# Optimization experiments

Measured on AMD Instinct MI355X. Metric: run time of the kernel, lower is better.

The kernel has to match this reference:

```python
import jax, jax.numpy as jnp
import numpy as np


def _lstm_scan(x, W, U, b):
    """Unidirectional Keras-style LSTM over x: [B, T, F] -> [B, T, H].
    Gate order (i, f, c, o); sigmoid recurrent activation, tanh activation."""
    B = x.shape[0]
    H = U.shape[0]
    # Precompute input projections for all timesteps: [B, T, 4H]
    xp = jnp.einsum('btf,fg->btg', x, W) + b

    def step(carry, xt):
        h, c = carry
        z = xt + h @ U  # [B, 4H]
        i, f, g, o = jnp.split(z, 4, axis=-1)
        i = jax.nn.sigmoid(i)
        f = jax.nn.sigmoid(f)
        g = jnp.tanh(g)
        o = jax.nn.sigmoid(o)
        c = f * c + i * g
        h = o * jnp.tanh(c)
        return (h, c), h

    init = (jnp.zeros((B, H), x.dtype), jnp.zeros((B, H), x.dtype))
    _, hs = jax.lax.scan(step, init, xp.transpose(1, 0, 2))  # [T, B, H]
    return hs.transpose(1, 0, 2)


def _bidir(x, Wf, Uf, bf, Wb, Ub, bb):
    fwd = _lstm_scan(x, Wf, Uf, bf)
    bwd = jnp.flip(_lstm_scan(jnp.flip(x, axis=1), Wb, Ub, bb), axis=1)
    return jnp.concatenate([fwd, bwd], axis=-1)  # merge_mode='concat'


def setup_inputs() -> dict:
    key = jax.random.key(0)
    ks = jax.random.split(key, 16)
    B, T, F, H = 64, 1024, 64, 256
    s_in0 = 1.0 / np.sqrt(F)
    s_in1 = 1.0 / np.sqrt(2 * H)
    s_rec = 1.0 / np.sqrt(H)
    inp = {
        'x': jax.random.normal(ks[0], (B, T, F), jnp.float32),
        'W0f': jax.random.normal(ks[1], (F, 4 * H), jnp.float32) * s_in0,
        'U0f': jax.random.normal(ks[2], (H, 4 * H), jnp.float32) * s_rec,
        'b0f': jnp.zeros((4 * H,), jnp.float32),
        'W0b': jax.random.normal(ks[3], (F, 4 * H), jnp.float32) * s_in0,
        'U0b': jax.random.normal(ks[4], (H, 4 * H), jnp.float32) * s_rec,
        'b0b': jnp.zeros((4 * H,), jnp.float32),
        'W1f': jax.random.normal(ks[5], (2 * H, 4 * H), jnp.float32) * s_in1,
        'U1f': jax.random.normal(ks[6], (H, 4 * H), jnp.float32) * s_rec,
        'b1f': jnp.zeros((4 * H,), jnp.float32),
        'W1b': jax.random.normal(ks[7], (2 * H, 4 * H), jnp.float32) * s_in1,
        'U1b': jax.random.normal(ks[8], (H, 4 * H), jnp.float32) * s_rec,
        'b1b': jnp.zeros((4 * H,), jnp.float32),
        'Wd': jax.random.normal(ks[9], (2 * H, 1), jnp.float32) * s_in1,
        'bd': jnp.zeros((1,), jnp.float32),
    }
    return inp


def reference(x, W0f, U0f, b0f, W0b, U0b, b0b,
              W1f, U1f, b1f, W1b, U1b, b1b, Wd, bd):
    # Layer 0 bidirectional LSTM -> [B, T, 2H]; dropout is identity at inference
    h = _bidir(x, W0f, U0f, b0f, W0b, U0b, b0b)
    # Layer 1 bidirectional LSTM -> [B, T, 2H]
    h = _bidir(h, W1f, U1f, b1f, W1b, U1b, b1b)
    # Dense(1, linear) head -> [B, T, 1]
    return jnp.einsum('btd,do->bto', h, Wd) + bd
```

## Files before the change

kernel.cpp:

```cpp
#include <hip/hip_runtime.h>
#include <hip/hip_bf16.h>
#include <cstdint>
#include <cstddef>

#define B_ 64
#define T_ 1024

typedef _Float16 half_t;
typedef __attribute__((ext_vector_type(8))) _Float16 half8;
typedef __attribute__((ext_vector_type(4))) float f32x4;
typedef __attribute__((ext_vector_type(8))) unsigned short ushort8;

__device__ __forceinline__ float sigm(float x) { return 1.f / (1.f + __expf(-x)); }
__device__ __forceinline__ float tanh_fast(float x) {
  float e = __expf(2.f * x);
  return 1.f - 2.f / (e + 1.f);
}

__global__ __launch_bounds__(256) void permute_cols(const float* __restrict__ src,
                                                    float* __restrict__ dst, int K) {
  int idx = blockIdx.x * 256 + threadIdx.x;
  if (idx >= K * 1024) return;
  int n = idx & 1023;
  size_t k = (size_t)(idx >> 10);
  dst[idx] = src[(k << 10) + ((size_t)(n & 3) << 8) + (n >> 2)];
}

__global__ __launch_bounds__(256) void pack_u_mfma(const float* __restrict__ src,
                                                   half_t* __restrict__ dst) {
  int tid = blockIdx.x * 256 + threadIdx.x;
  int l = tid & 63;
  int s = (tid >> 6) & 7;
  int n = (tid >> 9) & 1;
  int w = (tid >> 10) & 3;
  int wgc = (tid >> 12) & 7;
  int col = wgc * 128 + w * 32 + n * 16 + (l & 15);
  int hc = col >> 2, g = col & 3;
  int k0 = s * 32 + (l >> 4) * 8;
  half8 v;
#pragma unroll
  for (int j = 0; j < 8; ++j)
    v[j] = (half_t)src[(size_t)(k0 + j) * 1024 + (g << 8) + hc];
  *(half8*)(dst + (size_t)tid * 8) = v;
}

__global__ __launch_bounds__(256) void pack_w0_mfma(const float* __restrict__ src,
                                                    half_t* __restrict__ dst) {
  int line = blockIdx.x * 256 + threadIdx.x;
  int l = line & 63;
  int ks = (line >> 6) & 1;
  int n = (line >> 7) & 1;
  int w = (line >> 8) & 3;
  int wgc = (line >> 10) & 7;
  int col = wgc * 128 + w * 32 + n * 16 + (l & 15);
  int sc = ((col & 3) << 8) + (col >> 2);
  int k0 = ks * 32 + (l >> 4) * 8;
  half8 v;
#pragma unroll
  for (int j = 0; j < 8; ++j)
    v[j] = (half_t)src[(size_t)(k0 + j) * 1024 + sc];
  *(half8*)(dst + (size_t)line * 8) = v;
}

__global__ __launch_bounds__(256) void pack_w1_mfma(const float* __restrict__ src,
                                                    half_t* __restrict__ dst) {
  int tid = blockIdx.x * 256 + threadIdx.x;
  int l = tid & 63;
  int ks = (tid >> 6) & 15;
  int nb = tid >> 10;
  int colp = nb * 16 + (l & 15);
  int sc = ((colp & 3) << 8) + (colp >> 2);
  int k0 = ks * 32 + (l >> 4) * 8;
  half8 v;
#pragma unroll
  for (int j = 0; j < 8; ++j)
    v[j] = (half_t)src[(size_t)(k0 + j) * 1024 + sc];
  *(half8*)(dst + (size_t)tid * 8) = v;
}

__global__ __launch_bounds__(256) void pack_x_f16(const float* __restrict__ x,
                                                  unsigned short* __restrict__ xi) {
  int idx = blockIdx.x * 256 + threadIdx.x;
  int b = idx & 15;
  int q = (idx >> 4) & 3;
  int ks = (idx >> 6) & 1;
  int t = (idx >> 7) & 1023;
  int bg = idx >> 17;
  const float* src = x + ((size_t)(bg * 16 + b) * T_ + t) * 64 + ks * 32 + q * 8;
  ushort8 v;
#pragma unroll
  for (int j = 0; j < 8; ++j) {
    half_t h = (half_t)src[j];
    v[j] = __builtin_bit_cast(unsigned short, h);
  }
  *(ushort8*)(xi + (size_t)idx * 8) = v;
}

__global__ __launch_bounds__(256) void init_out(float* __restrict__ out,
                                                const float* __restrict__ bd, int n) {
  int i = blockIdx.x * 256 + threadIdx.x;
  if (i < n) out[i] = bd[0];
}

__global__ __launch_bounds__(256) void diag_out(float* __restrict__ out, int n, float v) {
  int i = blockIdx.x * 256 + threadIdx.x;
  if (i < n) out[i] = (i == 0) ? v : 0.f;
}

__global__ __launch_bounds__(256) void proj1_mfma(
    const unsigned short* __restrict__ h0,
    const half_t* __restrict__ Wf, const half_t* __restrict__ Wb,
    const float* __restrict__ bpf, const float* __restrict__ bpb,
    float* __restrict__ xp, int s0, int Tc) {
  const int dir = blockIdx.z;
  const half_t* Wpk = dir ? Wb : Wf;
  const float* bs = dir ? bpb : bpf;
  const int b = blockIdx.y;
  const int mt = blockIdx.x;
  const int tid = threadIdx.x;
  const int l = tid & 63, w = tid >> 6;

  __shared__ __align__(16) unsigned short A_lds[16][520];

  {
    int r = tid >> 4, c16 = tid & 15;
    int sl = mt * 16 + r;
    int t = dir ? (T_ - 1 - s0 - sl) : (s0 + sl);
    const ushort8* srcp =
        (const ushort8*)(h0 + ((size_t)b * T_ + t) * 512 + c16 * 32);
#pragma unroll
    for (int u = 0; u < 4; ++u)
      *(ushort8*)&A_lds[r][c16 * 32 + u * 8] = srcp[u];
  }
  __syncthreads();

  f32x4 acc[16];
#pragma unroll
  for (int n = 0; n < 16; ++n) acc[n] = (f32x4){0.f, 0.f, 0.f, 0.f};

  for (int ks = 0; ks < 16; ++ks) {
    half8 a = *(const half8*)&A_lds[l & 15][ks * 32 + (l >> 4) * 8];
    const half_t* bp_ = Wpk + (((size_t)(w * 16) * 16 + ks) * 64 + l) * 8;
#pragma unroll
    for (int n = 0; n < 16; ++n) {
      half8 bfr = *(const half8*)(bp_ + (size_t)n * 16 * 64 * 8);
      acc[n] = __builtin_amdgcn_mfma_f32_16x16x32_f16(a, bfr, acc[n], 0, 0, 0);
    }
  }

#pragma unroll
  for (int n = 0; n < 16; ++n) {
    int col = (w * 16 + n) * 16 + (l & 15);
    float bias = bs[col];
#pragma unroll
    for (int r = 0; r < 4; ++r) {
      int sl = mt * 16 + (l >> 4) * 4 + r;
      xp[(((size_t)dir * B_ + b) * Tc + sl) * 1024 + col] = acc[n][r] + bias;
    }
  }
}

template <int L0>
__global__ __launch_bounds__(256, 1) void lstm_scan_mfma(
    const float* __restrict__ xp,
    const unsigned short* __restrict__ xi,
    const half_t* __restrict__ W0f_, const half_t* __restrict__ W0b_,
    const float* __restrict__ b0f_, const float* __restrict__ b0b_,
    const half_t* __restrict__ Upk_f, const half_t* __restrict__ Upk_b,
    float* __restrict__ carry_c,
    unsigned* __restrict__ payl, unsigned* __restrict__ flagw,
    int s0, int Tc, int tagbase,
    unsigned short* __restrict__ hout,
    const float* __restrict__ Wd, float* __restrict__ out) {
  const int blk = blockIdx.x;
  const int unit = blk & 7;
  const int wgc = blk >> 3;
  const int dir = unit & 1;
  const int bg = unit >> 1;
  const int b0u = bg * 16;
  const int tid = threadIdx.x;
  const int l = tid & 63;
  const int w = tid >> 6;

  __shared__ __align__(16) unsigned short A_lds[4096];
  __shared__ __align__(16) unsigned short hstage[512];
  __shared__ float red_sm[64];

  const half_t* Upk = dir ? Upk_b : Upk_f;
  half8 U[2][8];
  {
    const half_t* up = Upk + (size_t)(wgc * 4 + w) * 8192;
#pragma unroll
    for (int n = 0; n < 2; ++n)
#pragma unroll
      for (int s = 0; s < 8; ++s)
        U[n][s] = *(const half8*)(up + ((size_t)(n * 8 + s) * 64 + l) * 8);
  }

  const int b_lane = 4 * (l >> 4) + (l & 3);
  const int hcb = wgc * 32 + w * 8 + ((l >> 2) & 3);
  const int colb = wgc * 128 + w * 32 + (l & 15);
  float cst[2];
#pragma unroll
  for (int n = 0; n < 2; ++n)
    cst[n] = (s0 == 0) ? 0.f
        : carry_c[((size_t)dir * B_ + b0u + b_lane) * 256 + hcb + n * 4];

  float wdl[2] = {0.f, 0.f};
  half8 W0r[2][2];
  float bias0[2] = {0.f, 0.f};
  const unsigned short* xib = nullptr;
  if (L0) {
    const half_t* W0pk = dir ? W0b_ : W0f_;
    const float* bs0 = dir ? b0b_ : b0f_;
#pragma unroll
    for (int n = 0; n < 2; ++n) {
      bias0[n] = bs0[colb + n * 16];
#pragma unroll
      for (int ks = 0; ks < 2; ++ks)
        W0r[n][ks] = *(const half8*)(W0pk +
            ((size_t)(((wgc * 4 + w) * 2 + n) * 2 + ks) * 64 + l) * 8);
    }
    xib = xi + (size_t)bg * T_ * 1024;
  } else {
    wdl[0] = Wd[dir * 256 + hcb];
    wdl[1] = Wd[dir * 256 + hcb + 4];
  }

  unsigned* payl_u = payl + (size_t)unit * 4096;
  unsigned* flag_u = flagw + unit * 16;

  if (s0 == 0) {
#pragma unroll
    for (int i = 0; i < 8; ++i) ((unsigned*)A_lds)[tid * 8 + i] = 0u;
  } else {
    unsigned dd[8];
#pragma unroll
    for (int i = 0; i < 8; ++i)
      dd[i] = __hip_atomic_load(payl_u + 2048 + tid * 8 + i,
                                __ATOMIC_RELAXED, __HIP_MEMORY_SCOPE_AGENT);
#pragma unroll
    for (int i = 0; i < 8; ++i)
      ((unsigned*)A_lds)[tid * 8 + i] = dd[i];
  }
  __syncthreads();

  const float* xpu = L0 ? nullptr : (xp + (size_t)(dir * B_ + b0u) * Tc * 1024);

  float xpre[2][4];
  half8 xfre[2];
  {
    if (L0) {
      int t0f = dir ? (T_ - 1 - s0) : s0;
#pragma unroll
      for (int ks = 0; ks < 2; ++ks)
        xfre[ks] = *(const half8*)((const half_t*)xib + (size_t)t0f * 1024 +
                                   ((ks * 4 + (l >> 4)) * 16 + (l & 15)) * 8);
    } else {
#pragma unroll
      for (int n = 0; n < 2; ++n)
#pragma unroll
        for (int r = 0; r < 4; ++r)
          xpre[n][r] = xpu[((size_t)(4 * (l >> 4) + r) * Tc) * 1024 + colb + n * 16];
    }
  }

  const int hbl = (w * 16 + b_lane) * 8 + ((l >> 2) & 3);

  for (int sl = 0; sl < Tc; ++sl) {
    const int s = s0 + sl;
    const int t = dir ? (T_ - 1 - s) : s;
    const int slot = s & 1;

    f32x4 acc[2];
    if (L0) {
#pragma unroll
      for (int n = 0; n < 2; ++n)
#pragma unroll
        for (int r = 0; r < 4; ++r) acc[n][r] = bias0[n];
      half8 xa0 = xfre[0], xa1 = xfre[1];
#pragma unroll
      for (int n = 0; n < 2; ++n) {
        acc[n] = __builtin_amdgcn_mfma_f32_16x16x32_f16(xa0, W0r[n][0], acc[n], 0, 0, 0);
        acc[n] = __builtin_amdgcn_mfma_f32_16x16x32_f16(xa1, W0r[n][1], acc[n], 0, 0, 0);
      }
    } else {
#pragma unroll
      for (int n = 0; n < 2; ++n)
#pragma unroll
        for (int r = 0; r < 4; ++r) acc[n][r] = xpre[n][r];
    }

    half8 a[8];
#pragma unroll
    for (int sK = 0; sK < 8; ++sK)
      a[sK] = *(const half8*)&((const half_t*)A_lds)[((sK * 4 + (l >> 4)) * 16 + (l & 15)) * 8];

#pragma unroll
    for (int sK = 0; sK < 8; ++sK) {
      acc[0] = __builtin_amdgcn_mfma_f32_16x16x32_f16(a[sK], U[0][sK], acc[0], 0, 0, 0);
      acc[1] = __builtin_amdgcn_mfma_f32_16x16x32_f16(a[sK], U[1][sK], acc[1], 0, 0, 0);
    }

    float vhead = 0.f;
    unsigned short hu2[2];
#pragma unroll
    for (int n = 0; n < 2; ++n) {
      float v0 = acc[n][0], v1 = acc[n][1], v2 = acc[n][2], v3 = acc[n][3];
      float x0 = __shfl_xor(v1, 1), x1 = __shfl_xor(v0, 1);
      float x2 = __shfl_xor(v3, 1), x3 = __shfl_xor(v2, 1);
      float a0 = (l & 1) ? x0 : v0;
      float a1 = (l & 1) ? v1 : x1;
      float a2 = (l & 1) ? x2 : v2;
      float a3 = (l & 1) ? v3 : x3;
      float y0 = __shfl_xor(a2, 2), y1 = __shfl_xor(a3, 2);
      float y2 = __shfl_xor(a0, 2), y3 = __shfl_xor(a1, 2);
      float u0 = (l & 2) ? y0 : a0;
      float u1 = (l & 2) ? y1 : a1;
      float u2 = (l & 2) ? a2 : y2;
      float u3 = (l & 2) ? a3 : y3;

      float iG = sigm(u0), fG = sigm(u1), gG = tanh_fast(u2), oG = sigm(u3);
      float cn = fG * cst[n] + iG * gG;
      cst[n] = cn;
      float h = oG * tanh_fast(cn);

      if (!L0) vhead += h * wdl[n];
      hu2[n] = __builtin_bit_cast(unsigned short, (half_t)h);
      if (sl == Tc - 1)
        carry_c[((size_t)dir * B_ + b0u + b_lane) * 256 + hcb + n * 4] = cn;
    }
    hstage[hbl] = hu2[0];
    hstage[hbl + 4] = hu2[1];
    if (!L0) {
      vhead += __shfl_xor(vhead, 4);
      vhead += __shfl_xor(vhead, 8);
      if ((l & 12) == 0) red_sm[w * 16 + b_lane] = vhead;
    }
    __syncthreads();

    const unsigned* hs32 = (const unsigned*)hstage;
    __hip_atomic_store(payl_u + slot * 2048 + wgc * 256 + tid, hs32[tid],
                       __ATOMIC_RELAXED, __HIP_MEMORY_SCOPE_AGENT);

    asm volatile("s_waitcnt vmcnt(0)" ::: "memory");
    __syncthreads();
    const unsigned want = (unsigned)(tagbase + s + 1);
    if (tid == 0)
      __hip_atomic_store(flag_u + slot * 8 + wgc, want,
                         __ATOMIC_RELAXED, __HIP_MEMORY_SCOPE_AGENT);

    if (L0) {
      int bb = tid >> 4, cc = tid & 15;
      ((unsigned*)hout)[((size_t)(b0u + bb) * T_ + t) * 256 + dir * 128 +
                        wgc * 16 + cc] = hs32[(cc >> 2) * 64 + bb * 4 + (cc & 3)];
    } else if (tid < 16) {
      atomicAdd(out + (((size_t)(b0u + tid)) << 10) + t,
                (red_sm[tid] + red_sm[16 + tid]) +
                (red_sm[32 + tid] + red_sm[48 + tid]));
    }

    if (sl + 1 < Tc) {
      if (L0) {
        int tn = dir ? (T_ - 2 - s) : (s + 1);
#pragma unroll
        for (int ks = 0; ks < 2; ++ks)
          xfre[ks] = *(const half8*)((const half_t*)xib + (size_t)tn * 1024 +
                                     ((ks * 4 + (l >> 4)) * 16 + (l & 15)) * 8);
      } else {
#pragma unroll
        for (int n = 0; n < 2; ++n)
#pragma unroll
          for (int r = 0; r < 4; ++r)
            xpre[n][r] = xpu[((size_t)(4 * (l >> 4) + r) * Tc + sl + 1) * 1024 + colb + n * 16];
      }

      if (tid < 8 && tid != wgc) {
        while (__hip_atomic_load(flag_u + slot * 8 + tid, __ATOMIC_RELAXED,
                                 __HIP_MEMORY_SCOPE_AGENT) != want) {}
      }
      __syncthreads();
      unsigned dd[8];
      const int g = tid >> 5;
      if (g == wgc) {
#pragma unroll
        for (int i = 0; i < 8; ++i) dd[i] = hs32[(tid & 31) * 8 + i];
      } else {
#pragma unroll
        for (int i = 0; i < 8; ++i)
          dd[i] = __hip_atomic_load(payl_u + slot * 2048 + tid * 8 + i,
                                    __ATOMIC_RELAXED, __HIP_MEMORY_SCOPE_AGENT);
      }
#pragma unroll
      for (int i = 0; i < 8; ++i)
        ((unsigned*)A_lds)[tid * 8 + i] = dd[i];
      __syncthreads();
    }
  }
}

extern "C" void kernel_launch(void* const* d_in, const int* in_sizes, int n_in,
                              void* d_out, int out_size, void* d_ws, size_t ws_size,
                              hipStream_t stream) {
  const float* x   = (const float*)d_in[0];
  const float* W0f = (const float*)d_in[1];
  const float* U0f = (const float*)d_in[2];
  const float* b0f = (const float*)d_in[3];
  const float* W0b = (const float*)d_in[4];
  const float* U0b = (const float*)d_in[5];
  const float* b0b = (const float*)d_in[6];
  const float* W1f = (const float*)d_in[7];
  const float* U1f = (const float*)d_in[8];
  const float* b1f = (const float*)d_in[9];
  const float* W1b = (const float*)d_in[10];
  const float* U1b = (const float*)d_in[11];
  const float* b1b = (const float*)d_in[12];
  const float* Wd  = (const float*)d_in[13];
  const float* bd  = (const float*)d_in[14];
  float* out = (float*)d_out;
  char* ws = (char*)d_ws;

  const size_t H0_BYTES   = (size_t)B_ * T_ * 512 * 2;
  const size_t UPK_BYTES  = (size_t)262144 * 2;
  const size_t W0PK_BYTES = (size_t)8192 * 8 * 2;
  const size_t W1PK_BYTES = (size_t)512 * 1024 * 2;
  const size_t XI_BYTES   = (size_t)B_ * T_ * 64 * 2;
  const size_t BP_BYTES   = 1024 * 4;
  const size_t CC_BYTES   = (size_t)2 * B_ * 256 * 4;
  const size_t PL_BYTES   = (size_t)8 * 4096 * 4;
  const size_t FL_BYTES   = 1024;
  const size_t REPACK = 4 * UPK_BYTES + 2 * W0PK_BYTES + 2 * W1PK_BYTES +
                        XI_BYTES + 4 * BP_BYTES + CC_BYTES + PL_BYTES +
                        FL_BYTES + 1024;

  int Tc = 0;
  for (int tc = 256; tc >= 64; tc >>= 1) {
    size_t xpb = (size_t)2 * B_ * tc * 1024 * 4;
    if (H0_BYTES + REPACK + xpb <= ws_size) { Tc = tc; break; }
  }
  if (!Tc) {
    float v = 1000.f + (float)(ws_size >> 20);
    diag_out<<<(out_size + 255) / 256, 256, 0, stream>>>(out, out_size, v);
    return;
  }

  size_t off = 0;
  unsigned short* h0 = (unsigned short*)(ws + off); off += H0_BYTES;
  half_t* Up00 = (half_t*)(ws + off); off += UPK_BYTES;
  half_t* Up01 = (half_t*)(ws + off); off += UPK_BYTES;
  half_t* Up10 = (half_t*)(ws + off); off += UPK_BYTES;
  half_t* Up11 = (half_t*)(ws + off); off += UPK_BYTES;
  half_t* W0pf = (half_t*)(ws + off); off += W0PK_BYTES;
  half_t* W0pb = (half_t*)(ws + off); off += W0PK_BYTES;
  half_t* W1pf = (half_t*)(ws + off); off += W1PK_BYTES;
  half_t* W1pb = (half_t*)(ws + off); off += W1PK_BYTES;
  unsigned short* xi = (unsigned short*)(ws + off); off += XI_BYTES;
  float* bp0f = (float*)(ws + off); off += BP_BYTES;
  float* bp0b = (float*)(ws + off); off += BP_BYTES;
  float* bp1f = (float*)(ws + off); off += BP_BYTES;
  float* bp1b = (float*)(ws + off); off += BP_BYTES;
  float* carry_c = (float*)(ws + off); off += CC_BYTES;
  unsigned* payl = (unsigned*)(ws + off); off += PL_BYTES;
  unsigned* flagw = (unsigned*)(ws + off); off += FL_BYTES;
  off = (off + 255) & ~(size_t)255;
  float* xpc = (float*)(ws + off);

  pack_u_mfma<<<128, 256, 0, stream>>>(U0f, Up00);
  pack_u_mfma<<<128, 256, 0, stream>>>(U0b, Up01);
  pack_u_mfma<<<128, 256, 0, stream>>>(U1f, Up10);
  pack_u_mfma<<<128, 256, 0, stream>>>(U1b, Up11);
  pack_w0_mfma<<<32, 256, 0, stream>>>(W0f, W0pf);
  pack_w0_mfma<<<32, 256, 0, stream>>>(W0b, W0pb);
  pack_w1_mfma<<<256, 256, 0, stream>>>(W1f, W1pf);
  pack_w1_mfma<<<256, 256, 0, stream>>>(W1b, W1pb);
  pack_x_f16<<<2048, 256, 0, stream>>>(x, xi);
  permute_cols<<<4, 256, 0, stream>>>(b0f, bp0f, 1);
  permute_cols<<<4, 256, 0, stream>>>(b0b, bp0b, 1);
  permute_cols<<<4, 256, 0, stream>>>(b1f, bp1f, 1);
  permute_cols<<<4, 256, 0, stream>>>(b1b, bp1b, 1);

  lstm_scan_mfma<1><<<64, 256, 0, stream>>>(
      nullptr, xi, W0pf, W0pb, bp0f, bp0b, Up00, Up01, carry_c,
      payl, flagw, 0, T_, 0, h0, nullptr, nullptr);

  init_out<<<(out_size + 255) / 256, 256, 0, stream>>>(out, bd, out_size);
  const int nch = T_ / Tc;
  const dim3 pgrid(Tc / 16, B_, 2);
  for (int ci = 0; ci < nch; ++ci) {
    int s0c = ci * Tc;
    proj1_mfma<<<pgrid, 256, 0, stream>>>(h0, W1pf, W1pb, bp1f, bp1b,
                                          xpc, s0c, Tc);
    lstm_scan_mfma<0><<<64, 256, 0, stream>>>(
        xpc, nullptr, nullptr, nullptr, nullptr, nullptr, Up10, Up11, carry_c,
        payl, flagw, s0c, Tc, 1024, nullptr, Wd, out);
  }
}
```

Baseline: 6.721 ms.

## Replace flag-based cross-block handoff with tagged payload words polled directly

Each 16-bit hidden value is now published with the step tag in its upper half, inside a 64-bit atomic store, so consumers poll the payload words themselves instead of a separate flag. This drops the vmcnt wait, one __syncthreads and the flag store/spin round trip on every recurrent step. The cost is twice the payload traffic and buffer size, plus per-word polling loops in every consumer thread. Correctness relies on tags never colliding across slots and launches.

```diff
diff --git a/kernel.cpp b/kernel.cpp
--- a/kernel.cpp
+++ b/kernel.cpp
@@ -10,6 +10,7 @@
 typedef __attribute__((ext_vector_type(8))) _Float16 half8;
 typedef __attribute__((ext_vector_type(4))) float f32x4;
 typedef __attribute__((ext_vector_type(8))) unsigned short ushort8;
+typedef unsigned long long ull;
 
 __device__ __forceinline__ float sigm(float x) { return 1.f / (1.f + __expf(-x)); }
 __device__ __forceinline__ float tanh_fast(float x) {
@@ -168,7 +169,7 @@
     const float* __restrict__ b0f_, const float* __restrict__ b0b_,
     const half_t* __restrict__ Upk_f, const half_t* __restrict__ Upk_b,
     float* __restrict__ carry_c,
-    unsigned* __restrict__ payl, unsigned* __restrict__ flagw,
+    unsigned* __restrict__ payl,
     int s0, int Tc, int tagbase,
     unsigned short* __restrict__ hout,
     const float* __restrict__ Wd, float* __restrict__ out) {
@@ -227,21 +228,21 @@
     wdl[1] = Wd[dir * 256 + hcb + 4];
   }
 
-  unsigned* payl_u = payl + (size_t)unit * 4096;
-  unsigned* flag_u = flagw + unit * 16;
+  unsigned* payl_u = payl + (size_t)unit * 8192;
 
   if (s0 == 0) {
 #pragma unroll
     for (int i = 0; i < 8; ++i) ((unsigned*)A_lds)[tid * 8 + i] = 0u;
   } else {
-    unsigned dd[8];
+    unsigned tw[16];
+#pragma unroll
+    for (int i = 0; i < 16; ++i)
+      tw[i] = __hip_atomic_load(payl_u + 4096 + tid * 16 + i,
+                                __ATOMIC_RELAXED, __HIP_MEMORY_SCOPE_AGENT);
 #pragma unroll
     for (int i = 0; i < 8; ++i)
-      dd[i] = __hip_atomic_load(payl_u + 2048 + tid * 8 + i,
-                                __ATOMIC_RELAXED, __HIP_MEMORY_SCOPE_AGENT);
-#pragma unroll
-    for (int i = 0; i < 8; ++i)
-      ((unsigned*)A_lds)[tid * 8 + i] = dd[i];
+      ((unsigned*)A_lds)[tid * 8 + i] =
+          (tw[2 * i] & 0xFFFFu) | (tw[2 * i + 1] << 16);
   }
   __syncthreads();
 
@@ -340,15 +341,16 @@
     __syncthreads();
 
     const unsigned* hs32 = (const unsigned*)hstage;
-    __hip_atomic_store(payl_u + slot * 2048 + wgc * 256 + tid, hs32[tid],
-                       __ATOMIC_RELAXED, __HIP_MEMORY_SCOPE_AGENT);
-
-    asm volatile("s_waitcnt vmcnt(0)" ::: "memory");
-    __syncthreads();
     const unsigned want = (unsigned)(tagbase + s + 1);
-    if (tid == 0)
-      __hip_atomic_store(flag_u + slot * 8 + wgc, want,
-                         __ATOMIC_RELAXED, __HIP_MEMORY_SCOPE_AGENT);
+    {
+      unsigned h2 = hs32[tid];
+      unsigned w0 = (want << 16) | (h2 & 0xFFFFu);
+      unsigned w1 = (want << 16) | (h2 >> 16);
+      ull pub = ((ull)w1 << 32) | (ull)w0;
+      __hip_atomic_store(
+          (ull*)(payl_u + (size_t)slot * 4096 + wgc * 512 + tid * 2),
+          pub, __ATOMIC_RELAXED, __HIP_MEMORY_SCOPE_AGENT);
+    }
 
     if (L0) {
       int bb = tid >> 4, cc = tid & 15;
@@ -375,21 +377,33 @@
             xpre[n][r] = xpu[((size_t)(4 * (l >> 4) + r) * Tc + sl + 1) * 1024 + colb + n * 16];
       }
 
-      if (tid < 8 && tid != wgc) {
-        while (__hip_atomic_load(flag_u + slot * 8 + tid, __ATOMIC_RELAXED,
-                                 __HIP_MEMORY_SCOPE_AGENT) != want) {}
-      }
-      __syncthreads();
       unsigned dd[8];
       const int g = tid >> 5;
       if (g == wgc) {
 #pragma unroll
         for (int i = 0; i < 8; ++i) dd[i] = hs32[(tid & 31) * 8 + i];
       } else {
+        const unsigned* src = payl_u + (size_t)slot * 4096 + tid * 16;
+        unsigned tw[16];
+#pragma unroll
+        for (int i = 0; i < 16; ++i)
+          tw[i] = __hip_atomic_load(src + i, __ATOMIC_RELAXED,
+                                    __HIP_MEMORY_SCOPE_AGENT);
+        bool bad = true;
+        while (bad) {
+          bad = false;
+#pragma unroll
+          for (int i = 0; i < 16; ++i) {
+            if ((tw[i] >> 16) != want) {
+              tw[i] = __hip_atomic_load(src + i, __ATOMIC_RELAXED,
+                                        __HIP_MEMORY_SCOPE_AGENT);
+              bad = true;
+            }
+          }
+        }
 #pragma unroll
         for (int i = 0; i < 8; ++i)
-          dd[i] = __hip_atomic_load(payl_u + slot * 2048 + tid * 8 + i,
-                                    __ATOMIC_RELAXED, __HIP_MEMORY_SCOPE_AGENT);
+          dd[i] = (tw[2 * i] & 0xFFFFu) | (tw[2 * i + 1] << 16);
       }
 #pragma unroll
       for (int i = 0; i < 8; ++i)
@@ -427,11 +441,9 @@
   const size_t XI_BYTES   = (size_t)B_ * T_ * 64 * 2;
   const size_t BP_BYTES   = 1024 * 4;
   const size_t CC_BYTES   = (size_t)2 * B_ * 256 * 4;
-  const size_t PL_BYTES   = (size_t)8 * 4096 * 4;
-  const size_t FL_BYTES   = 1024;
+  const size_t PL_BYTES   = (size_t)8 * 8192 * 4;
   const size_t REPACK = 4 * UPK_BYTES + 2 * W0PK_BYTES + 2 * W1PK_BYTES +
-                        XI_BYTES + 4 * BP_BYTES + CC_BYTES + PL_BYTES +
-                        FL_BYTES + 1024;
+                        XI_BYTES + 4 * BP_BYTES + CC_BYTES + PL_BYTES + 1024;
 
   int Tc = 0;
   for (int tc = 256; tc >= 64; tc >>= 1) {
@@ -461,7 +473,6 @@
   float* bp1b = (float*)(ws + off); off += BP_BYTES;
   float* carry_c = (float*)(ws + off); off += CC_BYTES;
   unsigned* payl = (unsigned*)(ws + off); off += PL_BYTES;
-  unsigned* flagw = (unsigned*)(ws + off); off += FL_BYTES;
   off = (off + 255) & ~(size_t)255;
   float* xpc = (float*)(ws + off);
 
@@ -481,7 +492,7 @@
 
   lstm_scan_mfma<1><<<64, 256, 0, stream>>>(
       nullptr, xi, W0pf, W0pb, bp0f, bp0b, Up00, Up01, carry_c,
-      payl, flagw, 0, T_, 0, h0, nullptr, nullptr);
+      payl, 0, T_, 0, h0, nullptr, nullptr);
 
   init_out<<<(out_size + 255) / 256, 256, 0, stream>>>(out, bd, out_size);
   const int nch = T_ / Tc;
@@ -492,6 +503,6 @@
                                           xpc, s0c, Tc);
     lstm_scan_mfma<0><<<64, 256, 0, stream>>>(
         xpc, nullptr, nullptr, nullptr, nullptr, nullptr, Up10, Up11, carry_c,
-        payl, flagw, s0c, Tc, 1024, nullptr, Wd, out);
-  }
-}
+        payl, s0c, Tc, 1024, nullptr, Wd, out);
+  }
+}
```

New measurement: 7.992 ms. 18.9% more time.
